# Optimization experiments

Hardware: AMD Instinct MI355X
Metric: run time of the kernel (lower is better)

Reference implementation:

```python
import jax, jax.numpy as jnp
import numpy as np

NUM_SHEET = 16; MAX_W = 128; MAX_H = 128; MAX_P = 25; HIDDEN = 1024
CNN_DIM = 4 * NUM_SHEET * (MAX_W // 4) * (MAX_H // 4)
IN_DIM = CNN_DIM + 3 * MAX_P
ACT_DIM = 2 * NUM_SHEET * MAX_P


def setup_inputs():
    key = jax.random.key(0)
    ks = jax.random.split(key, 8)
    r = jax.random.randint(ks[0], (NUM_SHEET, MAX_W, MAX_H), 0, 20)
    stocks = jnp.where(r > 0, -1, 0).astype(jnp.int32)
    prod_sizes = jax.random.randint(ks[1], (MAX_P, 2), 1, 16).astype(jnp.int32)
    prod_qty = jax.random.randint(ks[2], (MAX_P,), 0, 10).astype(jnp.int32)
    def rnd(k, shape, scale):
        return jax.random.normal(k, shape, jnp.float32) * scale
    return {
        'stocks': stocks, 'prod_sizes': prod_sizes, 'prod_qty': prod_qty,
        'conv1_w': rnd(ks[3], (2, 1, 3, 3), 0.3), 'conv1_b': jnp.zeros((2,), jnp.float32),
        'conv2_w': rnd(ks[4], (4, 2, 3, 3), 0.2), 'conv2_b': jnp.zeros((4,), jnp.float32),
        'fc1_w': rnd(ks[5], (IN_DIM, HIDDEN), 0.004), 'fc1_b': jnp.zeros((HIDDEN,), jnp.float32),
        'fc2_w': rnd(ks[6], (HIDDEN, ACT_DIM), 0.03), 'fc2_b': jnp.zeros((ACT_DIM,), jnp.float32),
    }


def _valid_actions(stocks, sizes, qty):
    # Integral-image replacement for the O(sheet*product*W*H*w*h) nested-loop scan.
    filled = (stocks != -1).astype(jnp.int32)  # [S, W, H]
    ii = jnp.cumsum(jnp.cumsum(filled, axis=1), axis=2)
    ii = jnp.pad(ii, ((0, 0), (1, 0), (1, 0)))  # summed-area table [S, W+1, H+1]
    i = jnp.arange(MAX_W)[:, None]
    j = jnp.arange(MAX_H)[None, :]

    def fits(sat, wh):
        w, h = wh[0], wh[1]
        i2 = jnp.minimum(i + w, MAX_W)
        j2 = jnp.minimum(j + h, MAX_H)
        win = sat[i2, j2] - sat[i, j2] - sat[i2, j] + sat[i, j]  # filled count per window
        ok = (i <= MAX_W - w) & (j <= MAX_H - h)
        return jnp.any(ok & (win == 0))

    v0 = jax.vmap(lambda sat: jax.vmap(lambda wh: fits(sat, wh))(sizes))(ii)          # [S, P]
    v1 = jax.vmap(lambda sat: jax.vmap(lambda wh: fits(sat, wh[::-1]))(sizes))(ii)    # rotated
    v1 = v1 & ~v0  # original breaks out of the orientation loop once m=0 is valid
    have = (qty > 0)[None, :]
    valid = jnp.stack([v0 & have, v1 & have], axis=-1)  # [S, P, 2] -> index (s*P+p)*2+m
    return valid.reshape(-1)


def reference(stocks, prod_sizes, prod_qty, conv1_w, conv1_b, conv2_w, conv2_b, fc1_w, fc1_b, fc2_w, fc2_b):
    # preprocess: 1.0 where empty (-1); batch the per-sheet conv loop over the sheet axis
    x = (stocks == -1).astype(jnp.float32)[:, None]  # [S, 1, W, H]
    dn = ('NCHW', 'OIHW', 'NCHW')
    x = jax.nn.relu(jax.lax.conv_general_dilated(x, conv1_w, (2, 2), ((1, 1), (1, 1)), dimension_numbers=dn) + conv1_b[None, :, None, None])
    x = jax.nn.relu(jax.lax.conv_general_dilated(x, conv2_w, (2, 2), ((1, 1), (1, 1)), dimension_numbers=dn) + conv2_b[None, :, None, None])
    cnn_out = x.reshape(1, -1)  # per-sheet flatten then concat == sheet-major reshape
    pf = jnp.concatenate([prod_sizes.astype(jnp.float32), prod_qty.astype(jnp.float32)[:, None]], axis=1).reshape(1, -1)  # [1, 3P]
    combined = jnp.concatenate([cnn_out, pf], axis=1)  # [1, IN_DIM]
    h = jax.nn.relu(combined @ fc1_w + fc1_b)
    logits = h @ fc2_w + fc2_b  # [1, ACT_DIM]
    valid = _valid_actions(stocks, prod_sizes, prod_qty)
    logits = jnp.where(valid[None, :], logits, jnp.float32(-1e9))
    return jax.nn.softmax(logits, axis=1)
```

## Files before the change

kernel.cpp:

```cpp
#include <hip/hip_runtime.h>
#include <hip/hip_bf16.h>
#include <cstdint>

#define NSHEET 16
#define MAXW 128
#define MAXH 128
#define MAXP 25
#define HIDDEN 1024
#define CNN_DIM 65536
#define IN_DIM 65611
#define ACT_DIM 800
#define CHUNK 64
#define NCHUNK 1026
#define NVALID 800
#define FC2_BLOCKS 32

typedef float f32x4 __attribute__((ext_vector_type(4)));

#define OFF_COMB 0
#define OFF_SAT  262656
#define OFF_P1   786944
#define OFF_FITS 4989440
#define OFF_P2   4992640
#define OFF_CNT  5095040

__global__ __launch_bounds__(256) void k1_prep(
        const int* __restrict__ stocks, const int* __restrict__ psz,
        const int* __restrict__ pq,
        const float* __restrict__ c1w, const float* __restrict__ c1b,
        const float* __restrict__ c2w, const float* __restrict__ c2b,
        float* __restrict__ comb, unsigned short* __restrict__ satg,
        int* __restrict__ cnt)
{
    __shared__ __align__(16) unsigned char smem[49664];
    const int tid = threadIdx.x;
    if (blockIdx.x == 0 && tid == 0) *cnt = 0;
    if (blockIdx.x < NSHEET) {
        const int s = blockIdx.x;
        unsigned char* xs = smem;
        float* o1 = (float*)(smem + 16384);
        float* wb = (float*)(smem + 16384 + 32768);
        const int* st = stocks + s * 16384;
        for (int k = 0; k < 64; ++k) {
            int idx = tid + k * 256;
            xs[idx] = (st[idx] == -1) ? 1 : 0;
        }
        if (tid < 96) {
            float v;
            if (tid < 18)      v = c1w[tid];
            else if (tid < 20) v = c1b[tid - 18];
            else if (tid < 92) v = c2w[tid - 20];
            else               v = c2b[tid - 92];
            wb[tid] = v;
        }
        __syncthreads();
        for (int k = 0; k < 32; ++k) {
            int idx = tid + k * 256;
            int oc = idx >> 12;
            int r = idx & 4095;
            int oy = r >> 6, ox = r & 63;
            float acc = wb[18 + oc];
            #pragma unroll
            for (int ky = 0; ky < 3; ++ky) {
                int iy = 2 * oy - 1 + ky;
                if (iy < 0 || iy > 127) continue;
                #pragma unroll
                for (int kx = 0; kx < 3; ++kx) {
                    int ix = 2 * ox - 1 + kx;
                    if (ix < 0 || ix > 127) continue;
                    acc += (float)xs[iy * 128 + ix] * wb[oc * 9 + ky * 3 + kx];
                }
            }
            o1[idx] = fmaxf(acc, 0.f);
        }
        __syncthreads();
        for (int k = 0; k < 16; ++k) {
            int idx = tid + k * 256;
            int oc = idx >> 10;
            int r = idx & 1023;
            int oy = r >> 5, ox = r & 31;
            float acc = wb[92 + oc];
            #pragma unroll
            for (int ic = 0; ic < 2; ++ic)
            #pragma unroll
            for (int ky = 0; ky < 3; ++ky) {
                int iy = 2 * oy - 1 + ky;
                if (iy < 0 || iy > 63) continue;
                #pragma unroll
                for (int kx = 0; kx < 3; ++kx) {
                    int ix = 2 * ox - 1 + kx;
                    if (ix < 0 || ix > 63) continue;
                    acc += o1[ic * 4096 + iy * 64 + ix] *
                           wb[20 + ((oc * 2 + ic) * 9 + ky * 3 + kx)];
                }
            }
            comb[s * 4096 + idx] = fmaxf(acc, 0.f);
        }
        if (s == 0 && tid < 3 * MAXP) {
            int p = tid / 3, r = tid - p * 3;
            comb[CNN_DIM + tid] = (float)(r < 2 ? psz[p * 2 + r] : pq[p]);
        }
    } else {
        const int s = blockIdx.x - NSHEET;
        unsigned short* sat = (unsigned short*)smem;
        const int* st = stocks + s * 16384;
        for (int k = 0; k < 64; ++k) {
            int idx = tid + k * 256;
            sat[(idx >> 7) * 132 + (idx & 127)] = (st[idx] != -1) ? 1 : 0;
        }
        __syncthreads();
        if (tid < 128) {
            int run = 0;
            for (int c = 0; c < 128; ++c) {
                run += sat[tid * 132 + c];
                sat[tid * 132 + c] = (unsigned short)run;
            }
        }
        __syncthreads();
        if (tid < 128) {
            int run = 0;
            for (int r = 0; r < 128; ++r) {
                run += sat[r * 132 + tid];
                sat[r * 132 + tid] = (unsigned short)run;
            }
        }
        __syncthreads();
        for (int k = 0; k < 64; ++k) {
            int idx = tid + k * 256;
            satg[s * 16384 + idx] = sat[(idx >> 7) * 132 + (idx & 127)];
        }
    }
}

__global__ __launch_bounds__(256) void k2_fc1_valid(
        const float* __restrict__ comb, const float* __restrict__ fc1w,
        const unsigned short* __restrict__ satg, const int* __restrict__ psz,
        float* __restrict__ part1, int* __restrict__ fits)
{
    const int tid = threadIdx.x;
    if (blockIdx.x < NCHUNK) {
        const int b = blockIdx.x;
        const int base = b * CHUNK;
        const int nr = min(CHUNK, IN_DIM - base);
        __shared__ float cval[CHUNK + 8];
        __shared__ int   cidx[CHUNK + 8];
        __shared__ int   tot;
        if (tid < 64) {
            float v = (tid < nr) ? comb[base + tid] : 0.f;
            bool nz = (v != 0.f);
            unsigned long long m = __ballot(nz);
            int pre = __popcll(m & ((1ull << tid) - 1ull));
            if (nz) { cval[pre] = v; cidx[pre] = base + tid; }
            if (tid == 0) {
                int t = __popcll(m);
                int tp = (t + 7) & ~7;
                for (int u = t; u < tp; ++u) { cval[u] = 0.f; cidx[u] = base; }
                tot = tp;
            }
        }
        __syncthreads();
        const int totp = tot;
        f32x4 acc = {0.f, 0.f, 0.f, 0.f};
        const f32x4* W4 = (const f32x4*)fc1w;
        if (totp > 0) {
            f32x4 g[8]; float cv[8];
            #pragma unroll
            for (int u = 0; u < 8; ++u) {
                g[u] = __builtin_nontemporal_load(W4 + (long)cidx[u] * 256 + tid);
                cv[u] = cval[u];
            }
            for (int i = 0; i < totp; i += 8) {
                const bool more = (i + 8) < totp;
                #pragma unroll
                for (int u = 0; u < 8; ++u) {
                    f32x4 w = g[u]; float c = cv[u];
                    if (more) {
                        int nx = i + 8 + u;
                        g[u] = __builtin_nontemporal_load(W4 + (long)cidx[nx] * 256 + tid);
                        cv[u] = cval[nx];
                    }
                    acc += w * c;
                }
            }
        }
        ((f32x4*)part1)[b * 256 + tid] = acc;
    } else {
        const int vb = blockIdx.x - NCHUNK;
        const int s = vb / 50, pm = vb - s * 50;
        const int p = pm >> 1, m = pm & 1;
        const int w = psz[p * 2 + m];
        const int h = psz[p * 2 + 1 - m];
        const unsigned short* S = satg + s * 16384;
        const int imax = MAXW - w, jmax = MAXH - h;
        __shared__ int found;
        if (tid == 0) found = 0;
        __syncthreads();
        int f = 0;
        for (int pos = tid; pos < 16384; pos += 256) {
            int i = pos >> 7, j = pos & 127;
            if (i <= imax && j <= jmax) {
                int i2 = i + w - 1, j2 = j + h - 1;
                int sum = (int)S[i2 * 128 + j2]
                        - (i ? (int)S[(i - 1) * 128 + j2] : 0)
                        - (j ? (int)S[i2 * 128 + (j - 1)] : 0)
                        + ((i && j) ? (int)S[(i - 1) * 128 + (j - 1)] : 0);
                if (sum == 0) f = 1;
            }
        }
        if (f) atomicOr(&found, 1);
        __syncthreads();
        if (tid == 0) fits[s * 50 + pm] = found;
    }
}

__global__ __launch_bounds__(256) void k3_fused(
        const float* __restrict__ part1, const float* __restrict__ fc1b,
        const float* __restrict__ fc2w, const float* __restrict__ fc2b,
        const int* __restrict__ fits, const int* __restrict__ pq,
        float* __restrict__ part2, int* __restrict__ cnt,
        float* __restrict__ out)
{
    const int b = blockIdx.x;
    const int tid = threadIdx.x;
    const int k0 = b * 32;
    __shared__ float red[8][33];
    __shared__ float hl[32];
    {
        const int l = tid & 31, g = tid >> 5;
        float s = 0.f;
        for (int c = g; c < NCHUNK; c += 8)
            s += part1[c * 1024 + k0 + l];
        red[g][l] = s;
    }
    __syncthreads();
    if (tid < 32) {
        float t = fc1b[k0 + tid];
        #pragma unroll
        for (int k = 0; k < 8; ++k) t += red[k][tid];
        hl[tid] = fmaxf(t, 0.f);
    }
    __syncthreads();
    const int a4 = tid * 4;
    if (a4 < ACT_DIM) {
        f32x4 acc = {0.f, 0.f, 0.f, 0.f};
        #pragma unroll 4
        for (int k = 0; k < 32; ++k) {
            float hv = hl[k];
            if (hv == 0.f) continue;
            f32x4 w = *(const f32x4*)(fc2w + (size_t)(k0 + k) * ACT_DIM + a4);
            acc += w * hv;
        }
        *(f32x4*)(part2 + b * ACT_DIM + a4) = acc;
    }
    __threadfence();
    __syncthreads();
    __shared__ int amLast;
    if (tid == 0) amLast = (atomicAdd(cnt, 1) == FC2_BLOCKS - 1);
    __syncthreads();
    if (!amLast) return;
    __threadfence();

    __shared__ float lg[ACT_DIM];
    __shared__ float red2[8];
    __shared__ float gval[2];
    for (int a = tid; a < ACT_DIM; a += 256) {
        float v = fc2b[a];
        #pragma unroll
        for (int c = 0; c < FC2_BLOCKS; ++c) v += part2[c * ACT_DIM + a];
        int m = a & 1, t2 = a >> 1;
        int p = t2 % 25, s = t2 / 25;
        int v0 = fits[s * 50 + p * 2];
        int v1 = fits[s * 50 + p * 2 + 1];
        bool valid = (m == 0 ? (v0 != 0) : (v1 != 0 && v0 == 0)) && (pq[p] > 0);
        lg[a] = valid ? v : -1e9f;
    }
    __syncthreads();
    float lm = -3e38f;
    for (int a = tid; a < ACT_DIM; a += 256) lm = fmaxf(lm, lg[a]);
    for (int off = 32; off >= 1; off >>= 1) lm = fmaxf(lm, __shfl_down(lm, off));
    if ((tid & 63) == 0) red2[tid >> 6] = lm;
    __syncthreads();
    if (tid == 0) {
        float m = red2[0];
        for (int w = 1; w < 4; ++w) m = fmaxf(m, red2[w]);
        gval[0] = m;
    }
    __syncthreads();
    const float gmax = gval[0];
    float ls = 0.f;
    for (int a = tid; a < ACT_DIM; a += 256) {
        float e = expf(lg[a] - gmax);
        lg[a] = e;
        ls += e;
    }
    for (int off = 32; off >= 1; off >>= 1) ls += __shfl_down(ls, off);
    if ((tid & 63) == 0) red2[tid >> 6] = ls;
    __syncthreads();
    if (tid == 0) gval[1] = red2[0] + red2[1] + red2[2] + red2[3];
    __syncthreads();
    const float inv = 1.f / gval[1];
    for (int a = tid; a < ACT_DIM; a += 256) out[a] = lg[a] * inv;
}

extern "C" void kernel_launch(void* const* d_in, const int* in_sizes, int n_in,
                              void* d_out, int out_size, void* d_ws, size_t ws_size,
                              hipStream_t stream) {
    const int*   stocks = (const int*)d_in[0];
    const int*   psz    = (const int*)d_in[1];
    const int*   pq     = (const int*)d_in[2];
    const float* c1w    = (const float*)d_in[3];
    const float* c1b    = (const float*)d_in[4];
    const float* c2w    = (const float*)d_in[5];
    const float* c2b    = (const float*)d_in[6];
    const float* fc1w   = (const float*)d_in[7];
    const float* fc1b   = (const float*)d_in[8];
    const float* fc2w   = (const float*)d_in[9];
    const float* fc2b   = (const float*)d_in[10];
    float* out = (float*)d_out;
    char*  ws  = (char*)d_ws;

    float*          comb  = (float*)(ws + OFF_COMB);
    unsigned short* satg  = (unsigned short*)(ws + OFF_SAT);
    float*          part1 = (float*)(ws + OFF_P1);
    int*            fitsp = (int*)(ws + OFF_FITS);
    float*          part2 = (float*)(ws + OFF_P2);
    int*            cntp  = (int*)(ws + OFF_CNT);

    hipLaunchKernelGGL(k1_prep, dim3(2 * NSHEET), dim3(256), 0, stream,
                       stocks, psz, pq, c1w, c1b, c2w, c2b, comb, satg, cntp);
    hipLaunchKernelGGL(k2_fc1_valid, dim3(NCHUNK + NVALID), dim3(256), 0, stream,
                       comb, fc1w, satg, psz, part1, fitsp);
    hipLaunchKernelGGL(k3_fused, dim3(FC2_BLOCKS), dim3(256), 0, stream,
                       part1, fc1b, fc2w, fc2b, fitsp, pq, part2, cntp, out);
}
```

Baseline: 488.4 us.

## Split hidden reduction into wide separate kernel and drop nontemporal fc1 loads

The reduction of fc1 partial sums across 1026 chunks moves out of the 32-block fc2 kernel into its own kernel of 64 blocks with 1024 threads each. That spreads the roughly 4 MB partial-sum read over more CUs. The fc2 kernel then only reads the finished hidden vector. The sparse fc1 weight gathers also switch from nontemporal loads to ordinary cached loads. This adds one kernel launch and a small extra global buffer.

Result: faster. 463.0 us (-5.2%).

```diff
diff --git a/kernel.cpp b/kernel.cpp
--- a/kernel.cpp
+++ b/kernel.cpp
@@ -20,9 +20,10 @@
 #define OFF_COMB 0
 #define OFF_SAT  262656
 #define OFF_P1   786944
-#define OFF_FITS 4989440
-#define OFF_P2   4992640
-#define OFF_CNT  5095040
+#define OFF_H    4989440
+#define OFF_FITS 4993536
+#define OFF_P2   4996736
+#define OFF_CNT  5099136
 
 __global__ __launch_bounds__(256) void k1_prep(
         const int* __restrict__ stocks, const int* __restrict__ psz,
@@ -166,7 +167,7 @@
             f32x4 g[8]; float cv[8];
             #pragma unroll
             for (int u = 0; u < 8; ++u) {
-                g[u] = __builtin_nontemporal_load(W4 + (long)cidx[u] * 256 + tid);
+                g[u] = W4[(long)cidx[u] * 256 + tid];
                 cv[u] = cval[u];
             }
             for (int i = 0; i < totp; i += 8) {
@@ -176,7 +177,7 @@
                     f32x4 w = g[u]; float c = cv[u];
                     if (more) {
                         int nx = i + 8 + u;
-                        g[u] = __builtin_nontemporal_load(W4 + (long)cidx[nx] * 256 + tid);
+                        g[u] = W4[(long)cidx[nx] * 256 + tid];
                         cv[u] = cval[nx];
                     }
                     acc += w * c;
@@ -213,32 +214,38 @@
     }
 }
 
-__global__ __launch_bounds__(256) void k3_fused(
+__global__ __launch_bounds__(1024) void k3a_hred(
         const float* __restrict__ part1, const float* __restrict__ fc1b,
-        const float* __restrict__ fc2w, const float* __restrict__ fc2b,
-        const int* __restrict__ fits, const int* __restrict__ pq,
-        float* __restrict__ part2, int* __restrict__ cnt,
-        float* __restrict__ out)
+        float* __restrict__ h)
+{
+    const int j0 = blockIdx.x * 16;
+    const int l = threadIdx.x & 15;
+    const int g = threadIdx.x >> 4;
+    float s = 0.f;
+    for (int c = g; c < NCHUNK; c += 64)
+        s += part1[c * 1024 + j0 + l];
+    __shared__ float red[64][17];
+    red[g][l] = s;
+    __syncthreads();
+    if (threadIdx.x < 16) {
+        float t = fc1b[j0 + threadIdx.x];
+        #pragma unroll 8
+        for (int k = 0; k < 64; ++k) t += red[k][threadIdx.x];
+        h[j0 + threadIdx.x] = fmaxf(t, 0.f);
+    }
+}
+
+__global__ __launch_bounds__(256) void k3b_fc2final(
+        const float* __restrict__ h, const float* __restrict__ fc2w,
+        const float* __restrict__ fc2b, const int* __restrict__ fits,
+        const int* __restrict__ pq, float* __restrict__ part2,
+        int* __restrict__ cnt, float* __restrict__ out)
 {
     const int b = blockIdx.x;
     const int tid = threadIdx.x;
     const int k0 = b * 32;
-    __shared__ float red[8][33];
     __shared__ float hl[32];
-    {
-        const int l = tid & 31, g = tid >> 5;
-        float s = 0.f;
-        for (int c = g; c < NCHUNK; c += 8)
-            s += part1[c * 1024 + k0 + l];
-        red[g][l] = s;
-    }
-    __syncthreads();
-    if (tid < 32) {
-        float t = fc1b[k0 + tid];
-        #pragma unroll
-        for (int k = 0; k < 8; ++k) t += red[k][tid];
-        hl[tid] = fmaxf(t, 0.f);
-    }
+    if (tid < 32) hl[tid] = h[k0 + tid];
     __syncthreads();
     const int a4 = tid * 4;
     if (a4 < ACT_DIM) {
@@ -322,6 +329,7 @@
     float*          comb  = (float*)(ws + OFF_COMB);
     unsigned short* satg  = (unsigned short*)(ws + OFF_SAT);
     float*          part1 = (float*)(ws + OFF_P1);
+    float*          hbuf  = (float*)(ws + OFF_H);
     int*            fitsp = (int*)(ws + OFF_FITS);
     float*          part2 = (float*)(ws + OFF_P2);
     int*            cntp  = (int*)(ws + OFF_CNT);
@@ -330,6 +338,8 @@
                        stocks, psz, pq, c1w, c1b, c2w, c2b, comb, satg, cntp);
     hipLaunchKernelGGL(k2_fc1_valid, dim3(NCHUNK + NVALID), dim3(256), 0, stream,
                        comb, fc1w, satg, psz, part1, fitsp);
-    hipLaunchKernelGGL(k3_fused, dim3(FC2_BLOCKS), dim3(256), 0, stream,
-                       part1, fc1b, fc2w, fc2b, fitsp, pq, part2, cntp, out);
-}
+    hipLaunchKernelGGL(k3a_hred, dim3(64), dim3(1024), 0, stream,
+                       part1, fc1b, hbuf);
+    hipLaunchKernelGGL(k3b_fc2final, dim3(FC2_BLOCKS), dim3(256), 0, stream,
+                       hbuf, fc2w, fc2b, fitsp, pq, part2, cntp, out);
+}
```
